# Performance work log

Measured on AMD Instinct MI355X. Metric: run time of the kernel, lower is better.

## Reference

```python
import jax, jax.numpy as jnp
import numpy as np
from jax import lax

DIM = 512; NUM_HEADS = 8; WS = 2; POOL = 3
HEAD_DIM = DIM // NUM_HEADS
L_HEADS = int(NUM_HEADS * 0.5); L_DIM = L_HEADS * HEAD_DIM
H_HEADS = NUM_HEADS - L_HEADS; H_DIM = H_HEADS * HEAD_DIM
SCALE = HEAD_DIM ** (-0.5)


def setup_inputs():
    key = jax.random.key(0)
    ks = jax.random.split(key, 8)
    B, Hh, Ww = 8, 64, 64
    N = Hh * Ww
    s = lambda fan: 1.0 / np.sqrt(fan)
    return {
        'x': jax.random.normal(ks[0], (B, N, DIM), jnp.float32),
        'H': Hh,
        'l_q_w': jax.random.normal(ks[1], (DIM, L_DIM), jnp.float32) * s(DIM),
        'l_kv_w': jax.random.normal(ks[2], (DIM, 2 * L_DIM), jnp.float32) * s(DIM),
        'l_proj_w': jax.random.normal(ks[3], (L_DIM, L_DIM), jnp.float32) * s(L_DIM),
        'l_proj_b': jax.random.normal(ks[4], (L_DIM,), jnp.float32) * 0.01,
        'h_qkv_w': jax.random.normal(ks[5], (DIM, H_DIM), jnp.float32) * s(DIM),
        'h_proj_w': jax.random.normal(ks[6], (H_DIM, H_DIM), jnp.float32) * s(H_DIM),
        'h_proj_b': jax.random.normal(ks[7], (H_DIM,), jnp.float32) * 0.01,
    }


def _avgpool3_same(x):
    # x: [M, ws, ws, C]; 3x3 avg pool, stride 1, pad 1, count_include_pad=False
    ssum = lax.reduce_window(x, jnp.float32(0.0), lax.add,
                             (1, POOL, POOL, 1), (1, 1, 1, 1),
                             ((0, 0), (1, 1), (1, 1), (0, 0)))
    ones = jnp.ones(x.shape[1:3], x.dtype)
    cnt = lax.reduce_window(ones, jnp.float32(0.0), lax.add,
                            (POOL, POOL), (1, 1), ((1, 1), (1, 1)))
    return ssum / cnt[None, :, :, None]


def _hifi(x, h_qkv_w, h_proj_w, h_proj_b):
    B, H, W, C = x.shape
    hg, wg = H // WS, W // WS
    x = x @ h_qkv_w  # [B,H,W,H_DIM]
    # partition into ws x ws windows: [B*hg*wg, ws, ws, H_DIM]
    xw = x.reshape(B, hg, WS, wg, WS, H_DIM).transpose(0, 1, 3, 2, 4, 5)
    xw = xw.reshape(B * hg * wg, WS, WS, H_DIM)
    xw = _avgpool3_same(xw) - xw
    xw = xw.reshape(B, hg, wg, WS, WS, H_DIM).transpose(0, 1, 3, 2, 4, 5)
    xw = xw.reshape(B, H, W, H_DIM)
    return xw @ h_proj_w + h_proj_b


def _lofi(x, l_q_w, l_kv_w, l_proj_w, l_proj_b):
    B, H, W, C = x.shape
    q = (x @ l_q_w).reshape(B, H * W, L_HEADS, HEAD_DIM).transpose(0, 2, 1, 3)
    # spatial reduction: avg pool ws stride ws -> [B, H/ws * W/ws, C]
    xp = x.reshape(B, H // WS, WS, W // WS, WS, C).mean(axis=(2, 4))
    xp = xp.reshape(B, -1, C)
    kv = (xp @ l_kv_w).reshape(B, -1, 2, L_HEADS, HEAD_DIM)
    k = kv[:, :, 0].transpose(0, 2, 1, 3)  # [B,h,M,d]
    v = kv[:, :, 1].transpose(0, 2, 1, 3)
    attn = jax.nn.softmax(jnp.einsum('bhnd,bhmd->bhnm', q, k) * SCALE, axis=-1)
    out = jnp.einsum('bhnm,bhmd->bhnd', attn, v)
    out = out.transpose(0, 2, 1, 3).reshape(B, H, W, L_DIM)
    return out @ l_proj_w + l_proj_b


def reference(x, H, l_q_w, l_kv_w, l_proj_w, l_proj_b, h_qkv_w, h_proj_w, h_proj_b):
    B, N, C = x.shape
    W = N // H
    xg = x.reshape(B, H, W, C)
    hi = _hifi(xg, h_qkv_w, h_proj_w, h_proj_b)
    lo = _lofi(xg, l_q_w, l_kv_w, l_proj_w, l_proj_b)
    out = jnp.concatenate([hi, lo], axis=-1)  # [B,H,W,C]
    return out.reshape(B, N, C)
```

## Files before the change

### kernel.cpp

```cpp
#include <hip/hip_runtime.h>

typedef __bf16 bf16x8 __attribute__((ext_vector_type(8)));
typedef float  f32x4  __attribute__((ext_vector_type(4)));
typedef unsigned int u32x4 __attribute__((ext_vector_type(4)));
typedef unsigned short u16x8 __attribute__((ext_vector_type(8)));
typedef unsigned short u16x4 __attribute__((ext_vector_type(4)));

__device__ __forceinline__ unsigned short f2bf(float f) {
    return __builtin_bit_cast(unsigned short, (__bf16)f);
}
__device__ __forceinline__ float bf2f(unsigned short s) {
    return (float)__builtin_bit_cast(__bf16, s);
}
__device__ __forceinline__ bf16x8 as_bf16x8(u32x4 v) {
    return __builtin_bit_cast(bf16x8, v);
}

#define AS1 __attribute__((address_space(1)))
#define AS3 __attribute__((address_space(3)))
__device__ __forceinline__ void gload_lds16(const void* g, void* l) {
    __builtin_amdgcn_global_load_lds((const AS1 void*)g, (AS3 void*)l, 16, 0, 0);
}


__global__ __launch_bounds__(256) void k_prep(
        const float* __restrict__ x,
        const float* __restrict__ h_qkv_w, const float* __restrict__ l_q_w,
        const float* __restrict__ l_kv_w, const float* __restrict__ h_proj_w,
        const float* __restrict__ l_proj_w,
        unsigned short* __restrict__ xb, unsigned short* __restrict__ xpb,
        unsigned short* __restrict__ wcatT, unsigned short* __restrict__ lkvT,
        unsigned short* __restrict__ hprojT, unsigned short* __restrict__ lprojT) {
    int blk = blockIdx.x;
    if (blk < 8192) {
        int t = blk * 256 + threadIdx.x;
        int row = t >> 6, c8 = (t & 63) << 3;
        int b = row >> 12, nn = row & 4095;
        int hh = nn >> 6, ww = nn & 63;
        int mp = (((b << 10) + ((hh >> 1) << 5) + (ww >> 1)) << 2) + ((hh & 1) << 1) + (ww & 1);
        const float* src = x + (size_t)row * 512 + c8;
        f32x4 v0 = *(const f32x4*)src;
        f32x4 v1 = *(const f32x4*)(src + 4);
        u16x8 o = { f2bf(v0[0]), f2bf(v0[1]), f2bf(v0[2]), f2bf(v0[3]),
                    f2bf(v1[0]), f2bf(v1[1]), f2bf(v1[2]), f2bf(v1[3]) };
        *(u16x8*)(xb + (size_t)mp * 512 + c8) = o;
    } else if (blk < 10240) {
        int t = (blk - 8192) * 256 + threadIdx.x;
        int r = t >> 6, c8 = (t & 63) << 3;
        int b = r >> 10, hw = r & 1023;
        int h2 = hw >> 5, w2 = hw & 31;
        const float* base = x + ((size_t)(b << 12) + (h2 << 7) + (w2 << 1)) * 512 + c8;
        u16x8 o;
#pragma unroll
        for (int half = 0; half < 2; half++) {
            f32x4 a0 = *(const f32x4*)(base + half * 4);
            f32x4 a1 = *(const f32x4*)(base + 512 + half * 4);
            f32x4 a2 = *(const f32x4*)(base + 64 * 512 + half * 4);
            f32x4 a3 = *(const f32x4*)(base + 65 * 512 + half * 4);
            f32x4 m = (a0 + a1 + a2 + a3) * 0.25f;
#pragma unroll
            for (int j = 0; j < 4; j++) o[half * 4 + j] = f2bf(m[j]);
        }
        *(u16x8*)(xpb + (size_t)r * 512 + c8) = o;
    } else {
        int i = (blk - 10240) * 256 + threadIdx.x;
        if (i < 262144) {
            int n = i >> 9, k = i & 511;
            float v = (n < 256) ? h_qkv_w[k * 256 + n] : l_q_w[k * 256 + (n - 256)];
            wcatT[i] = f2bf(v);
        } else if (i < 524288) {
            int j = i - 262144; int n = j >> 9, k = j & 511;
            lkvT[j] = f2bf(l_kv_w[k * 512 + n]);
        } else if (i < 589824) {
            int j = i - 524288; int n = j >> 8, k = j & 255;
            hprojT[j] = f2bf(h_proj_w[k * 256 + n]);
        } else {
            int j = i - 589824; int n = j >> 8, k = j & 255;
            lprojT[j] = f2bf(l_proj_w[k * 256 + n]);
        }
    }
}

__device__ __forceinline__ void mm_core(
        const unsigned short* __restrict__ A, const unsigned short* __restrict__ Bt,
        size_t row0, int col0, int K,
        unsigned short* As, unsigned short* Bs, f32x4 (&acc)[4][4]) {
    const int tid = threadIdx.x;
    const int wave = tid >> 6, lane = tid & 63;
    const int m16 = lane & 15, quad = lane >> 4;
    const int wr = wave >> 1, wc = wave & 1;
    const int srow = lane >> 2;
    const int scol = (lane & 3) * 8;
    const unsigned short* Ap0 = A + (row0 + wave * 32 + srow) * (size_t)K + scol;
    const unsigned short* Ap1 = Ap0 + (size_t)16 * K;
    const unsigned short* Bp0 = Bt + (size_t)(col0 + wave * 32 + srow) * K + scol;
    const unsigned short* Bp1 = Bp0 + (size_t)16 * K;
    unsigned short* Al0 = As + wave * 1024;
    unsigned short* Al1 = As + wave * 1024 + 512;
    unsigned short* Bl0 = Bs + wave * 1024;
    unsigned short* Bl1 = Bs + wave * 1024 + 512;

    for (int k0 = 0; k0 < K; k0 += 32) {
        __syncthreads();
        gload_lds16(Ap0 + k0, Al0);
        gload_lds16(Ap1 + k0, Al1);
        gload_lds16(Bp0 + k0, Bl0);
        gload_lds16(Bp1 + k0, Bl1);
        __syncthreads();
        bf16x8 af[4], bfr[4];
#pragma unroll
        for (int mi = 0; mi < 4; mi++)
            af[mi] = as_bf16x8(*(const u32x4*)(As + (wr * 64 + mi * 16 + m16) * 32 + quad * 8));
#pragma unroll
        for (int ni = 0; ni < 4; ni++)
            bfr[ni] = as_bf16x8(*(const u32x4*)(Bs + (wc * 64 + ni * 16 + m16) * 32 + quad * 8));
#pragma unroll
        for (int mi = 0; mi < 4; mi++)
#pragma unroll
            for (int ni = 0; ni < 4; ni++)
                acc[mi][ni] = __builtin_amdgcn_mfma_f32_16x16x32_bf16(af[mi], bfr[ni], acc[mi][ni], 0, 0, 0);
    }
}

__global__ __launch_bounds__(256, 2) void k_mm512(
        const unsigned short* __restrict__ xb, const unsigned short* __restrict__ xpb,
        const unsigned short* __restrict__ wcatT, const unsigned short* __restrict__ lkvT,
        unsigned short* __restrict__ dbuf, unsigned short* __restrict__ qbuf,
        unsigned short* __restrict__ kbuf, unsigned short* __restrict__ vT) {
    __shared__ __align__(16) unsigned short As[128 * 32];
    __shared__ __align__(16) unsigned short Bs[128 * 32];
    const int flat = blockIdx.x;
    const bool isg1 = flat < 1024;
    const unsigned short* A;
    const unsigned short* Bt;
    size_t row0; int col0;
    if (isg1) { A = xb;  Bt = wcatT; row0 = (size_t)(flat >> 2) * 128; col0 = (flat & 3) * 128; }
    else { int f = flat - 1024; A = xpb; Bt = lkvT; row0 = (size_t)(f >> 2) * 128; col0 = (f & 3) * 128; }

    f32x4 acc[4][4] = {};
    mm_core(A, Bt, row0, col0, 512, As, Bs, acc);

    const int tid = threadIdx.x;
    const int wave = tid >> 6, lane = tid & 63;
    const int m16 = lane & 15, quad = lane >> 4;
    const int wr = wave >> 1, wc = wave & 1;

    if (isg1) {
        if (col0 < 256) {
#pragma unroll
            for (int mi = 0; mi < 4; mi++)
#pragma unroll
                for (int ni = 0; ni < 4; ni++) {
                    const int col = col0 + wc * 64 + ni * 16 + m16;
                    const size_t mb = row0 + wr * 64 + mi * 16 + quad * 4;
                    float v0 = acc[mi][ni][0], v1 = acc[mi][ni][1];
                    float v2 = acc[mi][ni][2], v3 = acc[mi][ni][3];
                    float m = 0.25f * ((v0 + v1) + (v2 + v3));
                    dbuf[(mb + 0) * 256 + col] = f2bf(m - v0);
                    dbuf[(mb + 1) * 256 + col] = f2bf(m - v1);
                    dbuf[(mb + 2) * 256 + col] = f2bf(m - v2);
                    dbuf[(mb + 3) * 256 + col] = f2bf(m - v3);
                }
        } else {
#pragma unroll
            for (int mi = 0; mi < 4; mi++)
#pragma unroll
                for (int ni = 0; ni < 4; ni++) {
                    const int col = col0 - 256 + wc * 64 + ni * 16 + m16;
                    const size_t mb = row0 + wr * 64 + mi * 16 + quad * 4;
#pragma unroll
                    for (int r = 0; r < 4; r++)
                        qbuf[(mb + r) * 256 + col] = f2bf(acc[mi][ni][r]);
                }
        }
    } else {
        if (col0 < 256) {
#pragma unroll
            for (int mi = 0; mi < 4; mi++)
#pragma unroll
                for (int ni = 0; ni < 4; ni++) {
                    const int col = col0 + wc * 64 + ni * 16 + m16;
                    const size_t row = row0 + wr * 64 + mi * 16 + quad * 4;
#pragma unroll
                    for (int r = 0; r < 4; r++)
                        kbuf[(row + r) * 256 + col] = f2bf(acc[mi][ni][r]);
                }
        } else {
#pragma unroll
            for (int mi = 0; mi < 4; mi++)
#pragma unroll
                for (int ni = 0; ni < 4; ni++) {
                    const int d = col0 - 256 + wc * 64 + ni * 16 + m16;
                    const int hh = d >> 6, dd = d & 63;
                    const size_t kvg = row0 + wr * 64 + mi * 16 + quad * 4;
                    const int b = (int)(kvg >> 10), kv = (int)(kvg & 1023);
                    u16x4 pk = { f2bf(acc[mi][ni][0]), f2bf(acc[mi][ni][1]),
                                 f2bf(acc[mi][ni][2]), f2bf(acc[mi][ni][3]) };
                    *(u16x4*)(vT + (((size_t)(b * 4 + hh) * 64 + dd) << 10) + kv) = pk;
                }
        }
    }
}

__global__ __launch_bounds__(256, 2) void k_mmproj(
        const unsigned short* __restrict__ dbuf, const unsigned short* __restrict__ aout,
        const unsigned short* __restrict__ hprojT, const unsigned short* __restrict__ lprojT,
        const float* __restrict__ h_proj_b, const float* __restrict__ l_proj_b,
        float* __restrict__ out) {
    __shared__ __align__(16) unsigned short As[128 * 32];
    __shared__ __align__(16) unsigned short Bs[128 * 32];
    const int flat = blockIdx.x;
    const bool hi = flat < 512;
    const int f = flat & 511;
    const unsigned short* A  = hi ? dbuf : aout;
    const unsigned short* Bt = hi ? hprojT : lprojT;
    const float* bias = hi ? h_proj_b : l_proj_b;
    const int coloff = hi ? 0 : 256;
    const size_t row0 = (size_t)(f >> 1) * 128;
    const int col0 = (f & 1) * 128;

    f32x4 acc[4][4] = {};
    mm_core(A, Bt, row0, col0, 256, As, Bs, acc);

    const int tid = threadIdx.x;
    const int wave = tid >> 6, lane = tid & 63;
    const int m16 = lane & 15, quad = lane >> 4;
    const int wr = wave >> 1, wc = wave & 1;

#pragma unroll
    for (int mi = 0; mi < 4; mi++)
#pragma unroll
        for (int ni = 0; ni < 4; ni++) {
            const int col = col0 + wc * 64 + ni * 16 + m16;
            const float bv = bias[col];
            const size_t mb = row0 + wr * 64 + mi * 16 + quad * 4;
            const int widx = (int)(mb >> 2);
            const int b = widx >> 10, rem = widx & 1023;
            const int h2 = rem >> 5, w2 = rem & 31;
            const size_t nb = ((size_t)b << 12) + (h2 << 7) + (w2 << 1);
            float* op = out + nb * 512 + coloff + col;
            op[0]            = acc[mi][ni][0] + bv;
            op[512]          = acc[mi][ni][1] + bv;
            op[64 * 512]     = acc[mi][ni][2] + bv;
            op[65 * 512]     = acc[mi][ni][3] + bv;
        }
}

__global__ __launch_bounds__(256, 2) void k_attn(
        const unsigned short* __restrict__ qbuf,
        const unsigned short* __restrict__ kbuf,
        const unsigned short* __restrict__ vT,
        unsigned short* __restrict__ aout) {
    __shared__ __align__(16) unsigned short Kb[2][64 * 72];
    __shared__ __align__(16) unsigned short Vb[2][64 * 72];
    __shared__ __align__(16) unsigned short Pl[4][64 * 72];
    const int tid = threadIdx.x;
    const int wave = tid >> 6, lane = tid & 63;
    const int m16 = lane & 15, quad = lane >> 4;
    const int qtile = blockIdx.x, bh = blockIdx.y;
    const int b = bh >> 2, h = bh & 3;

    bf16x8 qf[4][2];
    const size_t qrow0 = (size_t)b * 4096 + qtile * 256 + wave * 64;
#pragma unroll
    for (int qh = 0; qh < 4; qh++) {
        const unsigned short* qp = qbuf + (qrow0 + qh * 16 + m16) * 256 + h * 64 + quad * 8;
        qf[qh][0] = as_bf16x8(*(const u32x4*)qp);
        qf[qh][1] = as_bf16x8(*(const u32x4*)(qp + 32));
    }

    f32x4 o[4][4] = {};
    float lp[4] = {0.f, 0.f, 0.f, 0.f};

    const int sr = tid >> 3;
    const int sc = tid & 7;
    const unsigned short* kg = kbuf + ((size_t)b * 1024) * 256 + h * 64 + sc * 8;
    const unsigned short* vg = vT + ((size_t)bh * 64) * 1024 + sc * 8;

    u32x4 s0 = *(const u32x4*)(kg + (size_t)sr * 256);
    u32x4 s1 = *(const u32x4*)(kg + (size_t)(sr + 32) * 256);
    u32x4 s2 = *(const u32x4*)(vg + (size_t)sr * 1024);
    u32x4 s3 = *(const u32x4*)(vg + (size_t)(sr + 32) * 1024);
    *(u32x4*)&Kb[0][sr * 72 + sc * 8] = s0;
    *(u32x4*)&Kb[0][(sr + 32) * 72 + sc * 8] = s1;
    *(u32x4*)&Vb[0][sr * 72 + sc * 8] = s2;
    *(u32x4*)&Vb[0][(sr + 32) * 72 + sc * 8] = s3;

    for (int it = 0; it < 16; ++it) {
        const int cur = it & 1, nxt = cur ^ 1;
        __syncthreads();
        if (it + 1 < 16) {
            const size_t kvb = (size_t)(it + 1) * 64;
            s0 = *(const u32x4*)(kg + (kvb + sr) * 256);
            s1 = *(const u32x4*)(kg + (kvb + sr + 32) * 256);
            s2 = *(const u32x4*)(vg + kvb + (size_t)sr * 1024);
            s3 = *(const u32x4*)(vg + kvb + (size_t)(sr + 32) * 1024);
        }

#pragma unroll
        for (int mt = 0; mt < 4; mt++) {
            const unsigned short* kp = &Kb[cur][(mt * 16 + m16) * 72 + quad * 8];
            const bf16x8 kf0 = as_bf16x8(*(const u32x4*)kp);
            const bf16x8 kf1 = as_bf16x8(*(const u32x4*)(kp + 32));
            f32x4 st[4] = {};
#pragma unroll
            for (int qh = 0; qh < 4; qh++) {
                st[qh] = __builtin_amdgcn_mfma_f32_16x16x32_bf16(kf0, qf[qh][0], st[qh], 0, 0, 0);
                st[qh] = __builtin_amdgcn_mfma_f32_16x16x32_bf16(kf1, qf[qh][1], st[qh], 0, 0, 0);
            }
#pragma unroll
            for (int qh = 0; qh < 4; qh++) {
                float p0 = __expf(st[qh][0] * 0.125f);
                float p1 = __expf(st[qh][1] * 0.125f);
                float p2 = __expf(st[qh][2] * 0.125f);
                float p3 = __expf(st[qh][3] * 0.125f);
                lp[qh] += (p0 + p1) + (p2 + p3);
                u16x4 pk = { f2bf(p0), f2bf(p1), f2bf(p2), f2bf(p3) };
                *(u16x4*)&Pl[wave][(qh * 16 + m16) * 72 + mt * 16 + quad * 4] = pk;
            }
        }
        asm volatile("s_waitcnt lgkmcnt(0)" ::: "memory");

        bf16x8 pf[4][2];
#pragma unroll
        for (int qh = 0; qh < 4; qh++) {
            const unsigned short* pp = &Pl[wave][(qh * 16 + m16) * 72 + quad * 8];
            pf[qh][0] = as_bf16x8(*(const u32x4*)pp);
            pf[qh][1] = as_bf16x8(*(const u32x4*)(pp + 32));
        }
#pragma unroll
        for (int nt = 0; nt < 4; nt++) {
            const unsigned short* vp = &Vb[cur][(nt * 16 + m16) * 72 + quad * 8];
            const bf16x8 vf0 = as_bf16x8(*(const u32x4*)vp);
            const bf16x8 vf1 = as_bf16x8(*(const u32x4*)(vp + 32));
#pragma unroll
            for (int qh = 0; qh < 4; qh++) {
                o[qh][nt] = __builtin_amdgcn_mfma_f32_16x16x32_bf16(pf[qh][0], vf0, o[qh][nt], 0, 0, 0);
                o[qh][nt] = __builtin_amdgcn_mfma_f32_16x16x32_bf16(pf[qh][1], vf1, o[qh][nt], 0, 0, 0);
            }
        }

        if (it + 1 < 16) {
            *(u32x4*)&Kb[nxt][sr * 72 + sc * 8] = s0;
            *(u32x4*)&Kb[nxt][(sr + 32) * 72 + sc * 8] = s1;
            *(u32x4*)&Vb[nxt][sr * 72 + sc * 8] = s2;
            *(u32x4*)&Vb[nxt][(sr + 32) * 72 + sc * 8] = s3;
        }
    }

#pragma unroll
    for (int qh = 0; qh < 4; qh++) {
        float l = lp[qh];
        l += __shfl_xor(l, 16);
        l += __shfl_xor(l, 32);
        f32x4 linv;
#pragma unroll
        for (int r = 0; r < 4; r++)
            linv[r] = __builtin_amdgcn_rcpf(__shfl(l, quad * 4 + r));
#pragma unroll
        for (int nt = 0; nt < 4; nt++)
#pragma unroll
            for (int r = 0; r < 4; r++)
                aout[(qrow0 + qh * 16 + quad * 4 + r) * 256 + h * 64 + nt * 16 + m16] =
                    f2bf(o[qh][nt][r] * linv[r]);
    }
}


extern "C" void kernel_launch(void* const* d_in, const int* in_sizes, int n_in,
                              void* d_out, int out_size, void* d_ws, size_t ws_size,
                              hipStream_t stream) {
    (void)in_sizes; (void)n_in; (void)out_size; (void)ws_size;
    const float* x        = (const float*)d_in[0];
    const float* l_q_w    = (const float*)d_in[2];
    const float* l_kv_w   = (const float*)d_in[3];
    const float* l_proj_w = (const float*)d_in[4];
    const float* l_proj_b = (const float*)d_in[5];
    const float* h_qkv_w  = (const float*)d_in[6];
    const float* h_proj_w = (const float*)d_in[7];
    const float* h_proj_b = (const float*)d_in[8];
    float* out = (float*)d_out;

    char* ws = (char*)d_ws;
    unsigned short* xb     = (unsigned short*)(ws);
    unsigned short* aout   = (unsigned short*)(ws);
    unsigned short* dbuf   = (unsigned short*)(ws + 33554432);
    unsigned short* qbuf   = (unsigned short*)(ws + 50331648);
    unsigned short* kbuf   = (unsigned short*)(ws + 67108864);
    unsigned short* vT     = (unsigned short*)(ws + 71303168);
    unsigned short* xpb    = (unsigned short*)(ws + 75497472);
    unsigned short* wcatT  = (unsigned short*)(ws + 83886080);
    unsigned short* lkvT   = (unsigned short*)(ws + 84410368);
    unsigned short* hprojT = (unsigned short*)(ws + 84934656);
    unsigned short* lprojT = (unsigned short*)(ws + 85065728);

    k_prep<<<12800, 256, 0, stream>>>(x, h_qkv_w, l_q_w, l_kv_w, h_proj_w, l_proj_w,
                                      xb, xpb, wcatT, lkvT, hprojT, lprojT);
    k_mm512<<<1280, 256, 0, stream>>>(xb, xpb, wcatT, lkvT, dbuf, qbuf, kbuf, vT);
    k_attn<<<dim3(16, 32), 256, 0, stream>>>(qbuf, kbuf, vT, aout);
    k_mmproj<<<1024, 256, 0, stream>>>(dbuf, aout, hprojT, lprojT, h_proj_b, l_proj_b, out);
}
```

Before: 256.0 us.

## Keep softmax probabilities in registers and feed PV MFMA directly, drop LDS staging

The attention kernel no longer writes the exponentiated scores to a per-wave LDS buffer and reads them back. The S accumulator layout of each 16x16 tile already matches the A-operand layout of the 16x16x16 bf16 MFMA, so P is packed to bf16 in registers and multiplied against V immediately, per key sub-tile. This removes the LDS round trip, the lgkmcnt wait and 36KB of shared memory, which could raise occupancy. The cost is twice as many half-width (K=16) MFMA instructions for the PV product and more, smaller V reads from LDS.

```diff
diff --git a/kernel.cpp b/kernel.cpp
--- a/kernel.cpp
+++ b/kernel.cpp
@@ -5,6 +5,7 @@
 typedef unsigned int u32x4 __attribute__((ext_vector_type(4)));
 typedef unsigned short u16x8 __attribute__((ext_vector_type(8)));
 typedef unsigned short u16x4 __attribute__((ext_vector_type(4)));
+typedef short i16x4 __attribute__((ext_vector_type(4)));
 
 __device__ __forceinline__ unsigned short f2bf(float f) {
     return __builtin_bit_cast(unsigned short, (__bf16)f);
@@ -253,7 +254,6 @@
         unsigned short* __restrict__ aout) {
     __shared__ __align__(16) unsigned short Kb[2][64 * 72];
     __shared__ __align__(16) unsigned short Vb[2][64 * 72];
-    __shared__ __align__(16) unsigned short Pl[4][64 * 72];
     const int tid = threadIdx.x;
     const int wave = tid >> 6, lane = tid & 63;
     const int m16 = lane & 15, quad = lane >> 4;
@@ -302,12 +302,14 @@
             const unsigned short* kp = &Kb[cur][(mt * 16 + m16) * 72 + quad * 8];
             const bf16x8 kf0 = as_bf16x8(*(const u32x4*)kp);
             const bf16x8 kf1 = as_bf16x8(*(const u32x4*)(kp + 32));
-            f32x4 st[4] = {};
+            f32x4 st[4];
 #pragma unroll
             for (int qh = 0; qh < 4; qh++) {
-                st[qh] = __builtin_amdgcn_mfma_f32_16x16x32_bf16(kf0, qf[qh][0], st[qh], 0, 0, 0);
-                st[qh] = __builtin_amdgcn_mfma_f32_16x16x32_bf16(kf1, qf[qh][1], st[qh], 0, 0, 0);
+                f32x4 z = {};
+                z = __builtin_amdgcn_mfma_f32_16x16x32_bf16(kf0, qf[qh][0], z, 0, 0, 0);
+                st[qh] = __builtin_amdgcn_mfma_f32_16x16x32_bf16(kf1, qf[qh][1], z, 0, 0, 0);
             }
+            i16x4 pa[4];
 #pragma unroll
             for (int qh = 0; qh < 4; qh++) {
                 float p0 = __expf(st[qh][0] * 0.125f);
@@ -316,27 +318,14 @@
                 float p3 = __expf(st[qh][3] * 0.125f);
                 lp[qh] += (p0 + p1) + (p2 + p3);
                 u16x4 pk = { f2bf(p0), f2bf(p1), f2bf(p2), f2bf(p3) };
-                *(u16x4*)&Pl[wave][(qh * 16 + m16) * 72 + mt * 16 + quad * 4] = pk;
+                pa[qh] = __builtin_bit_cast(i16x4, pk);
             }
-        }
-        asm volatile("s_waitcnt lgkmcnt(0)" ::: "memory");
-
-        bf16x8 pf[4][2];
-#pragma unroll
-        for (int qh = 0; qh < 4; qh++) {
-            const unsigned short* pp = &Pl[wave][(qh * 16 + m16) * 72 + quad * 8];
-            pf[qh][0] = as_bf16x8(*(const u32x4*)pp);
-            pf[qh][1] = as_bf16x8(*(const u32x4*)(pp + 32));
-        }
-#pragma unroll
-        for (int nt = 0; nt < 4; nt++) {
-            const unsigned short* vp = &Vb[cur][(nt * 16 + m16) * 72 + quad * 8];
-            const bf16x8 vf0 = as_bf16x8(*(const u32x4*)vp);
-            const bf16x8 vf1 = as_bf16x8(*(const u32x4*)(vp + 32));
-#pragma unroll
-            for (int qh = 0; qh < 4; qh++) {
-                o[qh][nt] = __builtin_amdgcn_mfma_f32_16x16x32_bf16(pf[qh][0], vf0, o[qh][nt], 0, 0, 0);
-                o[qh][nt] = __builtin_amdgcn_mfma_f32_16x16x32_bf16(pf[qh][1], vf1, o[qh][nt], 0, 0, 0);
+#pragma unroll
+            for (int nt = 0; nt < 4; nt++) {
+                const i16x4 vb = *(const i16x4*)&Vb[cur][(nt * 16 + m16) * 72 + mt * 16 + quad * 4];
+#pragma unroll
+                for (int qh = 0; qh < 4; qh++)
+                    o[qh][nt] = __builtin_amdgcn_mfma_f32_16x16x16bf16_1k(pa[qh], vb, o[qh][nt], 0, 0, 0);
             }
         }
 
```

Result: faster. 245.6 us (-4.1%).
